# Optimization experiments

Measured on AMD Instinct MI355X. Metric: run time of the kernel, lower is better.

Reference implementation:

```python
import jax, jax.numpy as jnp
import numpy as np

N_NODES = 50000
N_EDGES = 800000
N_GRAPHS = 256
DIMS = [64, 128, 256, 512]
GRU_H = 256


def _linit(key, shape, fan_in):
    lim = 1.0 / np.sqrt(fan_in)
    return jax.random.uniform(key, shape, jnp.float32, -lim, lim)


def setup_inputs() -> dict:
    key = jax.random.key(0)
    ks = jax.random.split(key, 24)
    x = jax.random.normal(ks[0], (N_NODES, DIMS[0]), jnp.float32)
    edge_index = jax.random.randint(ks[1], (2, N_EDGES), 0, N_NODES, jnp.int64)
    batch_idx = jnp.sort(jax.random.randint(ks[2], (N_NODES,), 0, N_GRAPHS, jnp.int64))
    inp = {"x": x, "edge_index": edge_index, "batch_idx": batch_idx}
    # GCN layer weights (stored [in, out]) and biases
    for i in range(3):
        inp[f"gcn_w{i}"] = _linit(ks[3 + i], (DIMS[i], DIMS[i + 1]), DIMS[i])
        inp[f"gcn_b{i}"] = jnp.zeros((DIMS[i + 1],), jnp.float32)
    # gate nn: Linear(512, 1)
    inp["gate_w"] = _linit(ks[6], (DIMS[3], 1), DIMS[3])
    inp["gate_b"] = jnp.zeros((1,), jnp.float32)
    # GRU: 2 layers, torch layout W_ih [3H, in], W_hh [3H, H]
    ins = [DIMS[3], GRU_H]
    for l in range(2):
        inp[f"gru_wih{l}"] = _linit(ks[7 + 4 * l], (3 * GRU_H, ins[l]), GRU_H)
        inp[f"gru_whh{l}"] = _linit(ks[8 + 4 * l], (3 * GRU_H, GRU_H), GRU_H)
        inp[f"gru_bih{l}"] = _linit(ks[9 + 4 * l], (3 * GRU_H,), GRU_H)
        inp[f"gru_bhh{l}"] = _linit(ks[10 + 4 * l], (3 * GRU_H,), GRU_H)
    # output proj: Linear(256, 512), torch layout [out, in]
    inp["proj_w"] = _linit(ks[15], (DIMS[3], GRU_H), GRU_H)
    inp["proj_b"] = jnp.zeros((DIMS[3],), jnp.float32)
    return inp


def _gcn_norm(edge_index, n_nodes):
    # add self-loops, symmetric normalization (PyG GCNConv default)
    loop = jnp.arange(n_nodes, dtype=edge_index.dtype)
    src = jnp.concatenate([edge_index[0], loop])
    dst = jnp.concatenate([edge_index[1], loop])
    deg = jax.ops.segment_sum(jnp.ones_like(dst, jnp.float32), dst, num_segments=n_nodes)
    dinv = jnp.where(deg > 0, jax.lax.rsqrt(jnp.maximum(deg, 1.0)), 0.0)
    norm = dinv[src] * dinv[dst]
    return src, dst, norm


def _gru_cell(xv, h, wih, whh, bih, bhh):
    gi = xv @ wih.T + bih
    gh = h @ whh.T + bhh
    ir, iz, inn = jnp.split(gi, 3, axis=-1)
    hr, hz, hn = jnp.split(gh, 3, axis=-1)
    r = jax.nn.sigmoid(ir + hr)
    z = jax.nn.sigmoid(iz + hz)
    n = jnp.tanh(inn + r * hn)
    return (1.0 - z) * n + z * h


def reference(x, edge_index, batch_idx,
              gcn_w0, gcn_b0, gcn_w1, gcn_b1, gcn_w2, gcn_b2,
              gate_w, gate_b,
              gru_wih0, gru_whh0, gru_bih0, gru_bhh0,
              gru_wih1, gru_whh1, gru_bih1, gru_bhh1,
              proj_w, proj_b):
    n = x.shape[0]
    src, dst, norm = _gcn_norm(edge_index, n)
    for w, b in ((gcn_w0, gcn_b0), (gcn_w1, gcn_b1), (gcn_w2, gcn_b2)):
        h = x @ w                                  # [N, out]
        msg = h[src] * norm[:, None]               # gather over edges
        x = jax.ops.segment_sum(msg, dst, num_segments=n) + b
        x = jax.nn.relu(x)
    # attentional aggregation: segment softmax over gate scores
    gate = (x @ gate_w + gate_b)[:, 0]             # [N]
    gmax = jax.ops.segment_max(gate, batch_idx, num_segments=N_GRAPHS)
    e = jnp.exp(gate - gmax[batch_idx])
    denom = jax.ops.segment_sum(e, batch_idx, num_segments=N_GRAPHS)
    alpha = e / denom[batch_idx]
    graph_emb = jax.ops.segment_sum(x * alpha[:, None], batch_idx, num_segments=N_GRAPHS)  # [G, 512]
    # 2-layer GRU with seq_len=1, h0=0
    h0 = jnp.zeros((N_GRAPHS, GRU_H), x.dtype)
    h1 = _gru_cell(graph_emb, h0, gru_wih0, gru_whh0, gru_bih0, gru_bhh0)
    h2 = _gru_cell(h1, h0, gru_wih1, gru_whh1, gru_bih1, gru_bhh1)
    return h2 @ proj_w.T + proj_b                  # [G, 512]
```

## Files before the change

kernel.cpp:

```cpp
#include <hip/hip_runtime.h>


#define N_GRAPHS 256
#define GRU_H 256
#define SCAN_CHUNK 2048

typedef __attribute__((ext_vector_type(8))) short short8;
typedef __attribute__((ext_vector_type(4))) float floatx4;

typedef unsigned short ushort_t;
typedef unsigned int uint_t;

__device__ __forceinline__ float bflo(uint_t u) { return __uint_as_float(u << 16); }
__device__ __forceinline__ float bfhi(uint_t u) { return __uint_as_float(u & 0xffff0000u); }
__device__ __forceinline__ uint_t f2bf(float f) {
    uint_t u = __float_as_uint(f);
    return (u + 0x7fffu + ((u >> 16) & 1u)) >> 16;
}
__device__ __forceinline__ uint_t pack2(float a, float b) {
    return f2bf(a) | (f2bf(b) << 16);
}


__global__ void k_hist(const int* __restrict__ dst, int* __restrict__ counts, int E) {
    int e = blockIdx.x * blockDim.x + threadIdx.x;
    if (e < E) atomicAdd(&counts[dst[e]], 1);
}

__global__ __launch_bounds__(256) void k_scan1(const int* __restrict__ counts,
                                               int* __restrict__ rowptr,
                                               int* __restrict__ bsums,
                                               float* __restrict__ dinv, int n) {
    int b = blockIdx.x, t = threadIdx.x;
    int base = b * SCAN_CHUNK + t * 8;
    int v[8];
    int s = 0;
#pragma unroll
    for (int j = 0; j < 8; ++j) {
        int i = base + j;
        int c = (i < n) ? counts[i] : 0;
        v[j] = s;
        s += c;
        if (i < n) dinv[i] = rsqrtf((float)(c + 1));
    }
    __shared__ int sd[256];
    sd[t] = s;
    __syncthreads();
    for (int off = 1; off < 256; off <<= 1) {
        int tmp = (t >= off) ? sd[t - off] : 0;
        __syncthreads();
        sd[t] += tmp;
        __syncthreads();
    }
    int texcl = sd[t] - s;
    if (t == 255) bsums[b] = sd[255];
#pragma unroll
    for (int j = 0; j < 8; ++j) {
        int i = base + j;
        if (i < n) rowptr[i] = texcl + v[j];
    }
}

__global__ void k_scan2(int* __restrict__ bsums, int nb, int* __restrict__ rowptr, int n) {
    if (threadIdx.x == 0 && blockIdx.x == 0) {
        int run = 0;
        for (int b = 0; b < nb; ++b) { int t = bsums[b]; bsums[b] = run; run += t; }
        rowptr[n] = run;
    }
}

__global__ __launch_bounds__(256) void k_scan3(int* __restrict__ rowptr,
                                               int* __restrict__ cursor,
                                               const int* __restrict__ bsums, int n) {
    int b = blockIdx.x, t = threadIdx.x;
    int base = b * SCAN_CHUNK + t * 8;
    int off = bsums[b];
#pragma unroll
    for (int j = 0; j < 8; ++j) {
        int i = base + j;
        if (i < n) { int r = rowptr[i] + off; rowptr[i] = r; cursor[i] = r; }
    }
}

__global__ void k_fill(const int* __restrict__ src, const int* __restrict__ dst,
                       int* __restrict__ cursor, int* __restrict__ col, int E) {
    int e = blockIdx.x * blockDim.x + threadIdx.x;
    if (e < E) {
        int pos = atomicAdd(&cursor[dst[e]], 1);
        col[pos] = src[e];
    }
}


__global__ void k_wt(const float* __restrict__ W, ushort_t* __restrict__ Wt,
                     int K, int Nout, int shift ) {
    int idx = blockIdx.x * blockDim.x + threadIdx.x;
    if (idx >= K * Nout) return;
    int k = idx >> shift;
    int n = idx & (Nout - 1);
    Wt[(size_t)n * K + k] = (ushort_t)f2bf(W[idx]);
}


__global__ void k_split(const float* __restrict__ src, ushort_t* __restrict__ hi,
                        ushort_t* __restrict__ lo, int L) {
    int i = blockIdx.x * blockDim.x + threadIdx.x;
    if (i >= L) return;
    float v = src[i];
    uint_t h = f2bf(v);
    hi[i] = (ushort_t)h;
    lo[i] = (ushort_t)f2bf(v - __uint_as_float(h << 16));
}


__global__ void k_prescale(const float4* __restrict__ x, const float* __restrict__ dinv,
                           uint4* __restrict__ xs, int N) {
    int idx = blockIdx.x * blockDim.x + threadIdx.x;
    int n = idx >> 3;
    if (n >= N) return;
    float dn = dinv[n];
    float4 v0 = x[idx * 2], v1 = x[idx * 2 + 1];
    uint4 o;
    o.x = pack2(v0.x * dn, v0.y * dn);
    o.y = pack2(v0.z * dn, v0.w * dn);
    o.z = pack2(v1.x * dn, v1.y * dn);
    o.w = pack2(v1.z * dn, v1.w * dn);
    xs[idx] = o;
}


__device__ __forceinline__ void acc8(float& a0, float& a1, float& a2, float& a3,
                                     float& a4, float& a5, float& a6, float& a7,
                                     const uint4& v) {
    a0 += bflo(v.x); a1 += bfhi(v.x); a2 += bflo(v.y); a3 += bfhi(v.y);
    a4 += bflo(v.z); a5 += bfhi(v.z); a6 += bflo(v.w); a7 += bfhi(v.w);
}

__global__ void k_gather_bf16(const uint4* __restrict__ xs, const int* __restrict__ rp,
                              const int* __restrict__ col, const float* __restrict__ dinv,
                              uint4* __restrict__ agg, int N, int shift ) {
    int idx = blockIdx.x * blockDim.x + threadIdx.x;
    int n = idx >> shift;
    if (n >= N) return;
    int c = idx & ((1 << shift) - 1);
    int C8 = 1 << shift;
    int a = rp[n], b = rp[n + 1];
    uint4 u = xs[(size_t)n * C8 + c];
    float a0 = bflo(u.x), a1 = bfhi(u.x), a2 = bflo(u.y), a3 = bfhi(u.y);
    float a4 = bflo(u.z), a5 = bfhi(u.z), a6 = bflo(u.w), a7 = bfhi(u.w);
    int k = a;
    for (; k + 8 <= b; k += 8) {
        int ci[8];
#pragma unroll
        for (int j = 0; j < 8; ++j) ci[j] = col[k + j];
        uint4 v[8];
#pragma unroll
        for (int j = 0; j < 8; ++j) v[j] = xs[(size_t)ci[j] * C8 + c];
#pragma unroll
        for (int j = 0; j < 8; ++j)
            acc8(a0, a1, a2, a3, a4, a5, a6, a7, v[j]);
    }
    for (; k + 4 <= b; k += 4) {
        int ci[4];
#pragma unroll
        for (int j = 0; j < 4; ++j) ci[j] = col[k + j];
        uint4 v[4];
#pragma unroll
        for (int j = 0; j < 4; ++j) v[j] = xs[(size_t)ci[j] * C8 + c];
#pragma unroll
        for (int j = 0; j < 4; ++j)
            acc8(a0, a1, a2, a3, a4, a5, a6, a7, v[j]);
    }
    for (; k < b; ++k) {
        uint4 v = xs[(size_t)col[k] * C8 + c];
        acc8(a0, a1, a2, a3, a4, a5, a6, a7, v);
    }
    float dn = dinv[n];
    uint4 o;
    o.x = pack2(a0 * dn, a1 * dn);
    o.y = pack2(a2 * dn, a3 * dn);
    o.z = pack2(a4 * dn, a5 * dn);
    o.w = pack2(a6 * dn, a7 * dn);
    agg[idx] = o;
}


__global__ __launch_bounds__(256) void k_gemm_mfma(
    const ushort_t* __restrict__ A, const ushort_t* __restrict__ Wt,
    const float* __restrict__ bias, const float* __restrict__ dinv,
    ushort_t* __restrict__ C, int M, int K, int Nout, int scale_out) {
    __shared__ ushort_t As[64 * 72];
    __shared__ ushort_t Bs[64 * 72];
    int tid = threadIdx.x;
    int wave = tid >> 6, lane = tid & 63;
    int quad = lane >> 4, lr = lane & 15;
    int wm = (wave & 1) * 32, wn = (wave >> 1) * 32;
    int bm = blockIdx.x * 64, bn = blockIdx.y * 64;

    floatx4 zero = {0.f, 0.f, 0.f, 0.f};
    floatx4 acc00 = zero, acc01 = zero, acc10 = zero, acc11 = zero;

    int r0 = tid >> 3,         ko0 = (tid & 7) * 8;
    int r1 = (tid + 256) >> 3, ko1 = ((tid + 256) & 7) * 8;

    for (int k0 = 0; k0 < K; k0 += 64) {
        int ar0 = min(bm + r0, M - 1);
        int ar1 = min(bm + r1, M - 1);
        uint4 av0 = *(const uint4*)(A + (size_t)ar0 * K + k0 + ko0);
        uint4 av1 = *(const uint4*)(A + (size_t)ar1 * K + k0 + ko1);
        uint4 bv0 = *(const uint4*)(Wt + (size_t)(bn + r0) * K + k0 + ko0);
        uint4 bv1 = *(const uint4*)(Wt + (size_t)(bn + r1) * K + k0 + ko1);
        __syncthreads();
        *(uint4*)&As[r0 * 72 + ko0] = av0;
        *(uint4*)&As[r1 * 72 + ko1] = av1;
        *(uint4*)&Bs[r0 * 72 + ko0] = bv0;
        *(uint4*)&Bs[r1 * 72 + ko1] = bv1;
        __syncthreads();
#pragma unroll
        for (int ks = 0; ks < 2; ++ks) {
            short8 af0 = *(short8*)&As[(wm + lr) * 72 + ks * 32 + quad * 8];
            short8 af1 = *(short8*)&As[(wm + 16 + lr) * 72 + ks * 32 + quad * 8];
            short8 bf0 = *(short8*)&Bs[(wn + lr) * 72 + ks * 32 + quad * 8];
            short8 bf1 = *(short8*)&Bs[(wn + 16 + lr) * 72 + ks * 32 + quad * 8];
            acc00 = __builtin_amdgcn_mfma_f32_16x16x32_bf16(af0, bf0, acc00, 0, 0, 0);
            acc01 = __builtin_amdgcn_mfma_f32_16x16x32_bf16(af0, bf1, acc01, 0, 0, 0);
            acc10 = __builtin_amdgcn_mfma_f32_16x16x32_bf16(af1, bf0, acc10, 0, 0, 0);
            acc11 = __builtin_amdgcn_mfma_f32_16x16x32_bf16(af1, bf1, acc11, 0, 0, 0);
        }
    }

#pragma unroll
    for (int mi = 0; mi < 2; ++mi) {
#pragma unroll
        for (int ni = 0; ni < 2; ++ni) {
            floatx4 acc = (mi == 0) ? (ni == 0 ? acc00 : acc01)
                                    : (ni == 0 ? acc10 : acc11);
            int col = bn + wn + ni * 16 + lr;
            float bcol = bias[col];
#pragma unroll
            for (int r = 0; r < 4; ++r) {
                int row = bm + wm + mi * 16 + quad * 4 + r;
                if (row < M) {
                    float v = acc[r] + bcol;
                    v = fmaxf(v, 0.0f);
                    if (scale_out) v *= dinv[row];
                    C[(size_t)row * Nout + col] = (ushort_t)f2bf(v);
                }
            }
        }
    }
}


__global__ __launch_bounds__(256) void k_gemm3(
    const ushort_t* __restrict__ Ahi, const ushort_t* __restrict__ Alo,
    const ushort_t* __restrict__ Whi, const ushort_t* __restrict__ Wlo,
    const float* __restrict__ bias, float* __restrict__ C,
    int M, int K, int Nout) {
    __shared__ ushort_t AsH[64 * 72];
    __shared__ ushort_t AsL[64 * 72];
    __shared__ ushort_t BsH[64 * 72];
    __shared__ ushort_t BsL[64 * 72];
    int tid = threadIdx.x;
    int wave = tid >> 6, lane = tid & 63;
    int quad = lane >> 4, lr = lane & 15;
    int wm = (wave & 1) * 32, wn = (wave >> 1) * 32;
    int bm = blockIdx.x * 64, bn = blockIdx.y * 64;

    floatx4 zero = {0.f, 0.f, 0.f, 0.f};
    floatx4 acc00 = zero, acc01 = zero, acc10 = zero, acc11 = zero;

    int r0 = tid >> 3,         ko0 = (tid & 7) * 8;
    int r1 = (tid + 256) >> 3, ko1 = ((tid + 256) & 7) * 8;

    for (int k0 = 0; k0 < K; k0 += 64) {
        int ar0 = min(bm + r0, M - 1);
        int ar1 = min(bm + r1, M - 1);
        size_t a0o = (size_t)ar0 * K + k0 + ko0, a1o = (size_t)ar1 * K + k0 + ko1;
        size_t b0o = (size_t)(bn + r0) * K + k0 + ko0, b1o = (size_t)(bn + r1) * K + k0 + ko1;
        uint4 ah0 = *(const uint4*)(Ahi + a0o), ah1 = *(const uint4*)(Ahi + a1o);
        uint4 al0 = *(const uint4*)(Alo + a0o), al1 = *(const uint4*)(Alo + a1o);
        uint4 bh0 = *(const uint4*)(Whi + b0o), bh1 = *(const uint4*)(Whi + b1o);
        uint4 bl0 = *(const uint4*)(Wlo + b0o), bl1 = *(const uint4*)(Wlo + b1o);
        __syncthreads();
        *(uint4*)&AsH[r0 * 72 + ko0] = ah0; *(uint4*)&AsH[r1 * 72 + ko1] = ah1;
        *(uint4*)&AsL[r0 * 72 + ko0] = al0; *(uint4*)&AsL[r1 * 72 + ko1] = al1;
        *(uint4*)&BsH[r0 * 72 + ko0] = bh0; *(uint4*)&BsH[r1 * 72 + ko1] = bh1;
        *(uint4*)&BsL[r0 * 72 + ko0] = bl0; *(uint4*)&BsL[r1 * 72 + ko1] = bl1;
        __syncthreads();
#pragma unroll
        for (int ks = 0; ks < 2; ++ks) {
            int a0i = (wm + lr) * 72 + ks * 32 + quad * 8;
            int a1i = (wm + 16 + lr) * 72 + ks * 32 + quad * 8;
            int b0i = (wn + lr) * 72 + ks * 32 + quad * 8;
            int b1i = (wn + 16 + lr) * 72 + ks * 32 + quad * 8;
            short8 afh0 = *(short8*)&AsH[a0i], afh1 = *(short8*)&AsH[a1i];
            short8 afl0 = *(short8*)&AsL[a0i], afl1 = *(short8*)&AsL[a1i];
            short8 bfh0 = *(short8*)&BsH[b0i], bfh1 = *(short8*)&BsH[b1i];
            short8 bfl0 = *(short8*)&BsL[b0i], bfl1 = *(short8*)&BsL[b1i];
            acc00 = __builtin_amdgcn_mfma_f32_16x16x32_bf16(afh0, bfh0, acc00, 0, 0, 0);
            acc00 = __builtin_amdgcn_mfma_f32_16x16x32_bf16(afh0, bfl0, acc00, 0, 0, 0);
            acc00 = __builtin_amdgcn_mfma_f32_16x16x32_bf16(afl0, bfh0, acc00, 0, 0, 0);
            acc01 = __builtin_amdgcn_mfma_f32_16x16x32_bf16(afh0, bfh1, acc01, 0, 0, 0);
            acc01 = __builtin_amdgcn_mfma_f32_16x16x32_bf16(afh0, bfl1, acc01, 0, 0, 0);
            acc01 = __builtin_amdgcn_mfma_f32_16x16x32_bf16(afl0, bfh1, acc01, 0, 0, 0);
            acc10 = __builtin_amdgcn_mfma_f32_16x16x32_bf16(afh1, bfh0, acc10, 0, 0, 0);
            acc10 = __builtin_amdgcn_mfma_f32_16x16x32_bf16(afh1, bfl0, acc10, 0, 0, 0);
            acc10 = __builtin_amdgcn_mfma_f32_16x16x32_bf16(afl1, bfh0, acc10, 0, 0, 0);
            acc11 = __builtin_amdgcn_mfma_f32_16x16x32_bf16(afh1, bfh1, acc11, 0, 0, 0);
            acc11 = __builtin_amdgcn_mfma_f32_16x16x32_bf16(afh1, bfl1, acc11, 0, 0, 0);
            acc11 = __builtin_amdgcn_mfma_f32_16x16x32_bf16(afl1, bfh1, acc11, 0, 0, 0);
        }
    }

#pragma unroll
    for (int mi = 0; mi < 2; ++mi) {
#pragma unroll
        for (int ni = 0; ni < 2; ++ni) {
            floatx4 acc = (mi == 0) ? (ni == 0 ? acc00 : acc01)
                                    : (ni == 0 ? acc10 : acc11);
            int col = bn + wn + ni * 16 + lr;
            float bcol = bias ? bias[col] : 0.0f;
#pragma unroll
            for (int r = 0; r < 4; ++r) {
                int row = bm + wm + mi * 16 + quad * 4 + r;
                if (row < M)
                    C[(size_t)row * Nout + col] = acc[r] + bcol;
            }
        }
    }
}


__global__ void k_gru_ep(const float* __restrict__ gi, const float* __restrict__ bih,
                         const float* __restrict__ bhh,
                         ushort_t* __restrict__ hhi, ushort_t* __restrict__ hlo, int G) {
    int idx = blockIdx.x * blockDim.x + threadIdx.x;
    int g = idx >> 8, j = idx & 255;
    if (g >= G) return;
    const float* row = gi + (size_t)g * 768;
    float ir = row[j]       + bih[j]       + bhh[j];
    float iz = row[j + 256] + bih[j + 256] + bhh[j + 256];
    float in = row[j + 512] + bih[j + 512];
    float r = 1.0f / (1.0f + expf(-ir));
    float z = 1.0f / (1.0f + expf(-iz));
    float nn = tanhf(in + r * bhh[j + 512]);
    float h = (1.0f - z) * nn;
    uint_t hi = f2bf(h);
    hhi[idx] = (ushort_t)hi;
    hlo[idx] = (ushort_t)f2bf(h - __uint_as_float(hi << 16));
}


__global__ void k_gate(const uint4* __restrict__ x, const float4* __restrict__ gw,
                       const float* __restrict__ gb, float* __restrict__ gate, int N) {
    int gid = blockIdx.x * blockDim.x + threadIdx.x;
    int wave = gid >> 6;
    int lane = gid & 63;
    if (wave >= N) return;
    uint4 u = x[(size_t)wave * 64 + lane];
    float4 w0 = gw[lane * 2], w1 = gw[lane * 2 + 1];
    float acc = bflo(u.x) * w0.x + bfhi(u.x) * w0.y + bflo(u.y) * w0.z + bfhi(u.y) * w0.w
              + bflo(u.z) * w1.x + bfhi(u.z) * w1.y + bflo(u.w) * w1.z + bfhi(u.w) * w1.w;
#pragma unroll
    for (int off = 32; off > 0; off >>= 1) acc += __shfl_down(acc, off, 64);
    if (lane == 0) gate[wave] = acc + gb[0];
}


__global__ void k_gstart(const int* __restrict__ batch, int* __restrict__ gstart,
                         int N, int G) {
    int g = blockIdx.x * blockDim.x + threadIdx.x;
    if (g > G) return;
    if (g == G) { gstart[G] = N; return; }
    int lo = 0, hi = N;
    while (lo < hi) {
        int mid = (lo + hi) >> 1;
        if (batch[mid] < g) lo = mid + 1; else hi = mid;
    }
    gstart[g] = lo;
}


__global__ __launch_bounds__(256) void k_softmax_emb(
    const uint_t* __restrict__ x , const float* __restrict__ gate,
    const int* __restrict__ gstart, float* __restrict__ emb) {
    int g = blockIdx.x;
    int s = gstart[g], e = gstart[g + 1];
    __shared__ float red[256];
    __shared__ float sal[256];
    int tid = threadIdx.x;
    float m = -INFINITY;
    for (int i = s + tid; i < e; i += 256) m = fmaxf(m, gate[i]);
    red[tid] = m; __syncthreads();
    for (int off = 128; off > 0; off >>= 1) {
        if (tid < off) red[tid] = fmaxf(red[tid], red[tid + off]);
        __syncthreads();
    }
    m = red[0]; __syncthreads();
    float ssum = 0.f;
    for (int i = s + tid; i < e; i += 256) ssum += expf(gate[i] - m);
    red[tid] = ssum; __syncthreads();
    for (int off = 128; off > 0; off >>= 1) {
        if (tid < off) red[tid] += red[tid + off];
        __syncthreads();
    }
    float denom = red[0];
    float inv = (denom > 0.f) ? 1.0f / denom : 0.0f;
    float acc0 = 0.f, acc1 = 0.f;
    for (int base = s; base < e; base += 256) {
        int i = base + tid;
        __syncthreads();
        sal[tid] = (i < e) ? expf(gate[i] - m) * inv : 0.0f;
        __syncthreads();
        int cnt = min(256, e - base);
        for (int k = 0; k < cnt; ++k) {
            float a = sal[k];
            uint_t u = x[(size_t)(base + k) * 256 + tid];
            acc0 += a * bflo(u);
            acc1 += a * bfhi(u);
        }
    }
    emb[(size_t)g * 512 + tid * 2]     = acc0;
    emb[(size_t)g * 512 + tid * 2 + 1] = acc1;
}


extern "C" void kernel_launch(void* const* d_in, const int* in_sizes, int n_in,
                              void* d_out, int out_size, void* d_ws, size_t ws_size,
                              hipStream_t stream) {
    const float* x       = (const float*)d_in[0];
    const int*   ei      = (const int*)d_in[1];
    const int*   batch   = (const int*)d_in[2];
    const float* w0      = (const float*)d_in[3];
    const float* b0      = (const float*)d_in[4];
    const float* w1      = (const float*)d_in[5];
    const float* b1      = (const float*)d_in[6];
    const float* w2      = (const float*)d_in[7];
    const float* b2      = (const float*)d_in[8];
    const float* gate_w  = (const float*)d_in[9];
    const float* gate_b  = (const float*)d_in[10];
    const float* wih0    = (const float*)d_in[11];
    const float* bih0    = (const float*)d_in[13];
    const float* bhh0    = (const float*)d_in[14];
    const float* wih1    = (const float*)d_in[15];
    const float* bih1    = (const float*)d_in[17];
    const float* bhh1    = (const float*)d_in[18];
    const float* pw      = (const float*)d_in[19];
    const float* pb      = (const float*)d_in[20];
    float* out = (float*)d_out;

    const int N = in_sizes[2];
    const int E = in_sizes[1] / 2;
    const int G = N_GRAPHS;

    char* base = (char*)d_ws;
    size_t off = 0;
    auto alloc = [&](size_t bytes) -> char* {
        char* p = base + off;
        off = (off + bytes + 255) & ~(size_t)255;
        return p;
    };
    ushort_t* bufA  = (ushort_t*)alloc((size_t)N * 512 * 2);
    ushort_t* bufB  = (ushort_t*)alloc((size_t)N * 512 * 2);
    float* dinv     = (float*)alloc((size_t)N * 4);
    float* gateArr  = (float*)alloc((size_t)N * 4);
    int*   counts   = (int*)alloc((size_t)(N + 1) * 4);
    int*   cursor   = (int*)alloc((size_t)(N + 1) * 4);
    int*   rowptr   = (int*)alloc((size_t)(N + 1) * 4);
    int*   bsums    = (int*)alloc((size_t)256 * 4);
    int*   col      = (int*)alloc((size_t)E * 4);
    int*   gstart   = (int*)alloc((size_t)(G + 1) * 4);
    float* emb      = (float*)alloc((size_t)G * 512 * 4);
    ushort_t* wt0   = (ushort_t*)alloc((size_t)128 * 64 * 2);
    ushort_t* wt1   = (ushort_t*)alloc((size_t)256 * 128 * 2);
    ushort_t* wt2   = (ushort_t*)alloc((size_t)512 * 256 * 2);
    ushort_t* ih0H  = (ushort_t*)alloc((size_t)768 * 512 * 2);
    ushort_t* ih0L  = (ushort_t*)alloc((size_t)768 * 512 * 2);
    ushort_t* ih1H  = (ushort_t*)alloc((size_t)768 * 256 * 2);
    ushort_t* ih1L  = (ushort_t*)alloc((size_t)768 * 256 * 2);
    ushort_t* pwH   = (ushort_t*)alloc((size_t)512 * 256 * 2);
    ushort_t* pwL   = (ushort_t*)alloc((size_t)512 * 256 * 2);
    ushort_t* embH  = (ushort_t*)alloc((size_t)G * 512 * 2);
    ushort_t* embL  = (ushort_t*)alloc((size_t)G * 512 * 2);
    ushort_t* h1H   = (ushort_t*)alloc((size_t)G * 256 * 2);
    ushort_t* h1L   = (ushort_t*)alloc((size_t)G * 256 * 2);
    ushort_t* h2H   = (ushort_t*)alloc((size_t)G * 256 * 2);
    ushort_t* h2L   = (ushort_t*)alloc((size_t)G * 256 * 2);
    float* gi       = (float*)alloc((size_t)G * 768 * 4);
    (void)ws_size; (void)n_in; (void)out_size;

    const int* src = ei;
    const int* dst = ei + E;

    const int nb = (N + SCAN_CHUNK - 1) / SCAN_CHUNK;

    hipMemsetAsync(counts, 0, (size_t)(N + 1) * 4, stream);
    k_hist<<<(E + 255) / 256, 256, 0, stream>>>(dst, counts, E);
    k_scan1<<<nb, 256, 0, stream>>>(counts, rowptr, bsums, dinv, N);
    k_scan2<<<1, 64, 0, stream>>>(bsums, nb, rowptr, N);
    k_scan3<<<nb, 256, 0, stream>>>(rowptr, cursor, bsums, N);
    k_fill<<<(E + 255) / 256, 256, 0, stream>>>(src, dst, cursor, col, E);
    k_wt<<<(64 * 128 + 255) / 256, 256, 0, stream>>>(w0, wt0, 64, 128, 7);
    k_wt<<<(128 * 256 + 255) / 256, 256, 0, stream>>>(w1, wt1, 128, 256, 8);
    k_wt<<<(256 * 512 + 255) / 256, 256, 0, stream>>>(w2, wt2, 256, 512, 9);
    k_split<<<(768 * 512 + 255) / 256, 256, 0, stream>>>(wih0, ih0H, ih0L, 768 * 512);
    k_split<<<(768 * 256 + 255) / 256, 256, 0, stream>>>(wih1, ih1H, ih1L, 768 * 256);
    k_split<<<(512 * 256 + 255) / 256, 256, 0, stream>>>(pw, pwH, pwL, 512 * 256);

    int mBlocks = (N + 63) / 64;

    k_prescale<<<(N * 8 + 255) / 256, 256, 0, stream>>>((const float4*)x, dinv, (uint4*)bufA, N);
    k_gather_bf16<<<(N * 8 + 255) / 256, 256, 0, stream>>>((const uint4*)bufA, rowptr, col, dinv, (uint4*)bufB, N, 3);
    k_gemm_mfma<<<dim3(mBlocks, 2), 256, 0, stream>>>(bufB, wt0, b0, dinv, bufA, N, 64, 128, 1);

    k_gather_bf16<<<(N * 16 + 255) / 256, 256, 0, stream>>>((const uint4*)bufA, rowptr, col, dinv, (uint4*)bufB, N, 4);
    k_gemm_mfma<<<dim3(mBlocks, 4), 256, 0, stream>>>(bufB, wt1, b1, dinv, bufA, N, 128, 256, 1);

    k_gather_bf16<<<(N * 32 + 255) / 256, 256, 0, stream>>>((const uint4*)bufA, rowptr, col, dinv, (uint4*)bufB, N, 5);
    k_gemm_mfma<<<dim3(mBlocks, 8), 256, 0, stream>>>(bufB, wt2, b2, dinv, bufA, N, 256, 512, 0);

    k_gate<<<(N * 64 + 255) / 256, 256, 0, stream>>>((const uint4*)bufA, (const float4*)gate_w, gate_b, gateArr, N);
    k_gstart<<<1, 512, 0, stream>>>(batch, gstart, N, G);
    k_softmax_emb<<<G, 256, 0, stream>>>((const uint_t*)bufA, gateArr, gstart, emb);

    k_split<<<(G * 512 + 255) / 256, 256, 0, stream>>>(emb, embH, embL, G * 512);
    k_gemm3<<<dim3(G / 64, 12), 256, 0, stream>>>(embH, embL, ih0H, ih0L, nullptr, gi, G, 512, 768);
    k_gru_ep<<<G, 256, 0, stream>>>(gi, bih0, bhh0, h1H, h1L, G);

    k_gemm3<<<dim3(G / 64, 12), 256, 0, stream>>>(h1H, h1L, ih1H, ih1L, nullptr, gi, G, 256, 768);
    k_gru_ep<<<G, 256, 0, stream>>>(gi, bih1, bhh1, h2H, h2L, G);

    k_gemm3<<<dim3(G / 64, 8), 256, 0, stream>>>(h2H, h2L, pwH, pwL, pb, out, G, 256, 512);
}
```

Before: 461.6 us.

## Fuse gate projection into last GEMM epilogue and merge small setup kernels

Computes the attention gate dot product inside the final GCN GEMM epilogue, reducing across lanes with shuffles and accumulating per-row partials into a zeroed gate array with atomics. The separate gate and graph-start kernels go away, with graph bounds found by binary search inside the softmax kernel, which now writes the hi/lo bf16 split directly. The scan's second pass is folded into the third, and the weight conversion and split launches are merged into single kernels, all to cut launch count and one re-read of the 50000x512 activation. In exchange the gate uses fp32 atomics (non-deterministic order), the gate bias is dropped on the assumption it cancels in the softmax, and the memset relies on the workspace layout placing gateArr before counts.

```diff
diff --git a/kernel.cpp b/kernel.cpp
--- a/kernel.cpp
+++ b/kernel.cpp
@@ -61,20 +61,25 @@
     }
 }
 
-__global__ void k_scan2(int* __restrict__ bsums, int nb, int* __restrict__ rowptr, int n) {
-    if (threadIdx.x == 0 && blockIdx.x == 0) {
-        int run = 0;
-        for (int b = 0; b < nb; ++b) { int t = bsums[b]; bsums[b] = run; run += t; }
-        rowptr[n] = run;
-    }
-}
-
 __global__ __launch_bounds__(256) void k_scan3(int* __restrict__ rowptr,
                                                int* __restrict__ cursor,
-                                               const int* __restrict__ bsums, int n) {
+                                               const int* __restrict__ bsums,
+                                               int n, int nb) {
     int b = blockIdx.x, t = threadIdx.x;
+    __shared__ int s_off;
+    if (t == 0) {
+        int off = 0, tot = 0;
+        for (int i = 0; i < nb; ++i) {
+            int v = bsums[i];
+            if (i < b) off += v;
+            tot += v;
+        }
+        s_off = off;
+        if (b == 0) rowptr[n] = tot;
+    }
+    __syncthreads();
+    int off = s_off;
     int base = b * SCAN_CHUNK + t * 8;
-    int off = bsums[b];
 #pragma unroll
     for (int j = 0; j < 8; ++j) {
         int i = base + j;
@@ -92,24 +97,40 @@
 }
 
 
-__global__ void k_wt(const float* __restrict__ W, ushort_t* __restrict__ Wt,
-                     int K, int Nout, int shift ) {
+__global__ void k_wt_all(const float* __restrict__ w0, const float* __restrict__ w1,
+                         const float* __restrict__ w2, ushort_t* __restrict__ wt0,
+                         ushort_t* __restrict__ wt1, ushort_t* __restrict__ wt2) {
     int idx = blockIdx.x * blockDim.x + threadIdx.x;
-    if (idx >= K * Nout) return;
-    int k = idx >> shift;
-    int n = idx & (Nout - 1);
-    Wt[(size_t)n * K + k] = (ushort_t)f2bf(W[idx]);
-}
-
-
-__global__ void k_split(const float* __restrict__ src, ushort_t* __restrict__ hi,
-                        ushort_t* __restrict__ lo, int L) {
-    int i = blockIdx.x * blockDim.x + threadIdx.x;
-    if (i >= L) return;
-    float v = src[i];
+    if (idx < 8192) {
+        int k = idx >> 7, n = idx & 127;
+        wt0[(size_t)n * 64 + k] = (ushort_t)f2bf(w0[idx]);
+    } else if (idx < 40960) {
+        int i = idx - 8192;
+        int k = i >> 8, n = i & 255;
+        wt1[(size_t)n * 128 + k] = (ushort_t)f2bf(w1[i]);
+    } else if (idx < 172032) {
+        int i = idx - 40960;
+        int k = i >> 9, n = i & 511;
+        wt2[(size_t)n * 256 + k] = (ushort_t)f2bf(w2[i]);
+    }
+}
+
+
+__global__ void k_split_all(const float* __restrict__ wih0, const float* __restrict__ wih1,
+                            const float* __restrict__ pw,
+                            ushort_t* __restrict__ h0, ushort_t* __restrict__ l0,
+                            ushort_t* __restrict__ h1, ushort_t* __restrict__ l1,
+                            ushort_t* __restrict__ h2, ushort_t* __restrict__ l2) {
+    int idx = blockIdx.x * blockDim.x + threadIdx.x;
+    const float* s; ushort_t* H; ushort_t* L; int i;
+    if (idx < 393216)      { s = wih0; H = h0; L = l0; i = idx; }
+    else if (idx < 589824) { s = wih1; H = h1; L = l1; i = idx - 393216; }
+    else if (idx < 720896) { s = pw;   H = h2; L = l2; i = idx - 589824; }
+    else return;
+    float v = s[i];
     uint_t h = f2bf(v);
-    hi[i] = (ushort_t)h;
-    lo[i] = (ushort_t)f2bf(v - __uint_as_float(h << 16));
+    H[i] = (ushort_t)h;
+    L[i] = (ushort_t)f2bf(v - __uint_as_float(h << 16));
 }
 
 
@@ -188,7 +209,8 @@
 __global__ __launch_bounds__(256) void k_gemm_mfma(
     const ushort_t* __restrict__ A, const ushort_t* __restrict__ Wt,
     const float* __restrict__ bias, const float* __restrict__ dinv,
-    ushort_t* __restrict__ C, int M, int K, int Nout, int scale_out) {
+    ushort_t* __restrict__ C, int M, int K, int Nout, int scale_out,
+    const float* __restrict__ gate_w, float* __restrict__ gateArr) {
     __shared__ ushort_t As[64 * 72];
     __shared__ ushort_t Bs[64 * 72];
     int tid = threadIdx.x;
@@ -229,6 +251,12 @@
         }
     }
 
+    float gwv[2] = {0.f, 0.f};
+    if (gate_w) {
+        gwv[0] = gate_w[bn + wn + lr];
+        gwv[1] = gate_w[bn + wn + 16 + lr];
+    }
+    float pg[2][4] = {};
 #pragma unroll
     for (int mi = 0; mi < 2; ++mi) {
 #pragma unroll
@@ -243,8 +271,26 @@
                 if (row < M) {
                     float v = acc[r] + bcol;
                     v = fmaxf(v, 0.0f);
+                    if (gate_w) pg[mi][r] += v * gwv[ni];
                     if (scale_out) v *= dinv[row];
                     C[(size_t)row * Nout + col] = (ushort_t)f2bf(v);
+                }
+            }
+        }
+    }
+    if (gate_w) {
+#pragma unroll
+        for (int mi = 0; mi < 2; ++mi) {
+#pragma unroll
+            for (int r = 0; r < 4; ++r) {
+                float p = pg[mi][r];
+                p += __shfl_down(p, 8, 16);
+                p += __shfl_down(p, 4, 16);
+                p += __shfl_down(p, 2, 16);
+                p += __shfl_down(p, 1, 16);
+                if (lr == 0) {
+                    int row = bm + wm + mi * 16 + quad * 4 + r;
+                    if (row < M) atomicAdd(&gateArr[row], p);
                 }
             }
         }
@@ -352,41 +398,20 @@
 }
 
 
-__global__ void k_gate(const uint4* __restrict__ x, const float4* __restrict__ gw,
-                       const float* __restrict__ gb, float* __restrict__ gate, int N) {
-    int gid = blockIdx.x * blockDim.x + threadIdx.x;
-    int wave = gid >> 6;
-    int lane = gid & 63;
-    if (wave >= N) return;
-    uint4 u = x[(size_t)wave * 64 + lane];
-    float4 w0 = gw[lane * 2], w1 = gw[lane * 2 + 1];
-    float acc = bflo(u.x) * w0.x + bfhi(u.x) * w0.y + bflo(u.y) * w0.z + bfhi(u.y) * w0.w
-              + bflo(u.z) * w1.x + bfhi(u.z) * w1.y + bflo(u.w) * w1.z + bfhi(u.w) * w1.w;
-#pragma unroll
-    for (int off = 32; off > 0; off >>= 1) acc += __shfl_down(acc, off, 64);
-    if (lane == 0) gate[wave] = acc + gb[0];
-}
-
-
-__global__ void k_gstart(const int* __restrict__ batch, int* __restrict__ gstart,
-                         int N, int G) {
-    int g = blockIdx.x * blockDim.x + threadIdx.x;
-    if (g > G) return;
-    if (g == G) { gstart[G] = N; return; }
-    int lo = 0, hi = N;
-    while (lo < hi) {
-        int mid = (lo + hi) >> 1;
-        if (batch[mid] < g) lo = mid + 1; else hi = mid;
-    }
-    gstart[g] = lo;
-}
-
-
 __global__ __launch_bounds__(256) void k_softmax_emb(
     const uint_t* __restrict__ x , const float* __restrict__ gate,
-    const int* __restrict__ gstart, float* __restrict__ emb) {
+    const int* __restrict__ batch, int N,
+    ushort_t* __restrict__ embH, ushort_t* __restrict__ embL) {
     int g = blockIdx.x;
-    int s = gstart[g], e = gstart[g + 1];
+    int s, e;
+    {
+        int lo = 0, hi = N;
+        while (lo < hi) { int mid = (lo + hi) >> 1; if (batch[mid] < g) lo = mid + 1; else hi = mid; }
+        s = lo;
+        lo = s; hi = N;
+        while (lo < hi) { int mid = (lo + hi) >> 1; if (batch[mid] < g + 1) lo = mid + 1; else hi = mid; }
+        e = lo;
+    }
     __shared__ float red[256];
     __shared__ float sal[256];
     int tid = threadIdx.x;
@@ -421,8 +446,13 @@
             acc1 += a * bfhi(u);
         }
     }
-    emb[(size_t)g * 512 + tid * 2]     = acc0;
-    emb[(size_t)g * 512 + tid * 2 + 1] = acc1;
+    int i0 = g * 512 + tid * 2;
+    uint_t h0 = f2bf(acc0);
+    uint_t h1 = f2bf(acc1);
+    embH[i0]     = (ushort_t)h0;
+    embH[i0 + 1] = (ushort_t)h1;
+    embL[i0]     = (ushort_t)f2bf(acc0 - __uint_as_float(h0 << 16));
+    embL[i0 + 1] = (ushort_t)f2bf(acc1 - __uint_as_float(h1 << 16));
 }
 
 
@@ -439,7 +469,6 @@
     const float* w2      = (const float*)d_in[7];
     const float* b2      = (const float*)d_in[8];
     const float* gate_w  = (const float*)d_in[9];
-    const float* gate_b  = (const float*)d_in[10];
     const float* wih0    = (const float*)d_in[11];
     const float* bih0    = (const float*)d_in[13];
     const float* bhh0    = (const float*)d_in[14];
@@ -470,8 +499,6 @@
     int*   rowptr   = (int*)alloc((size_t)(N + 1) * 4);
     int*   bsums    = (int*)alloc((size_t)256 * 4);
     int*   col      = (int*)alloc((size_t)E * 4);
-    int*   gstart   = (int*)alloc((size_t)(G + 1) * 4);
-    float* emb      = (float*)alloc((size_t)G * 512 * 4);
     ushort_t* wt0   = (ushort_t*)alloc((size_t)128 * 64 * 2);
     ushort_t* wt1   = (ushort_t*)alloc((size_t)256 * 128 * 2);
     ushort_t* wt2   = (ushort_t*)alloc((size_t)512 * 256 * 2);
@@ -495,36 +522,31 @@
 
     const int nb = (N + SCAN_CHUNK - 1) / SCAN_CHUNK;
 
-    hipMemsetAsync(counts, 0, (size_t)(N + 1) * 4, stream);
+    size_t zbytes = (size_t)((char*)counts - (char*)gateArr) + (size_t)(N + 1) * 4;
+    hipMemsetAsync(gateArr, 0, zbytes, stream);
+
     k_hist<<<(E + 255) / 256, 256, 0, stream>>>(dst, counts, E);
     k_scan1<<<nb, 256, 0, stream>>>(counts, rowptr, bsums, dinv, N);
-    k_scan2<<<1, 64, 0, stream>>>(bsums, nb, rowptr, N);
-    k_scan3<<<nb, 256, 0, stream>>>(rowptr, cursor, bsums, N);
+    k_scan3<<<nb, 256, 0, stream>>>(rowptr, cursor, bsums, N, nb);
     k_fill<<<(E + 255) / 256, 256, 0, stream>>>(src, dst, cursor, col, E);
-    k_wt<<<(64 * 128 + 255) / 256, 256, 0, stream>>>(w0, wt0, 64, 128, 7);
-    k_wt<<<(128 * 256 + 255) / 256, 256, 0, stream>>>(w1, wt1, 128, 256, 8);
-    k_wt<<<(256 * 512 + 255) / 256, 256, 0, stream>>>(w2, wt2, 256, 512, 9);
-    k_split<<<(768 * 512 + 255) / 256, 256, 0, stream>>>(wih0, ih0H, ih0L, 768 * 512);
-    k_split<<<(768 * 256 + 255) / 256, 256, 0, stream>>>(wih1, ih1H, ih1L, 768 * 256);
-    k_split<<<(512 * 256 + 255) / 256, 256, 0, stream>>>(pw, pwH, pwL, 512 * 256);
+    k_wt_all<<<(172032 + 255) / 256, 256, 0, stream>>>(w0, w1, w2, wt0, wt1, wt2);
+    k_split_all<<<(720896 + 255) / 256, 256, 0, stream>>>(wih0, wih1, pw,
+                                                          ih0H, ih0L, ih1H, ih1L, pwH, pwL);
 
     int mBlocks = (N + 63) / 64;
 
     k_prescale<<<(N * 8 + 255) / 256, 256, 0, stream>>>((const float4*)x, dinv, (uint4*)bufA, N);
     k_gather_bf16<<<(N * 8 + 255) / 256, 256, 0, stream>>>((const uint4*)bufA, rowptr, col, dinv, (uint4*)bufB, N, 3);
-    k_gemm_mfma<<<dim3(mBlocks, 2), 256, 0, stream>>>(bufB, wt0, b0, dinv, bufA, N, 64, 128, 1);
+    k_gemm_mfma<<<dim3(mBlocks, 2), 256, 0, stream>>>(bufB, wt0, b0, dinv, bufA, N, 64, 128, 1, nullptr, nullptr);
 
     k_gather_bf16<<<(N * 16 + 255) / 256, 256, 0, stream>>>((const uint4*)bufA, rowptr, col, dinv, (uint4*)bufB, N, 4);
-    k_gemm_mfma<<<dim3(mBlocks, 4), 256, 0, stream>>>(bufB, wt1, b1, dinv, bufA, N, 128, 256, 1);
+    k_gemm_mfma<<<dim3(mBlocks, 4), 256, 0, stream>>>(bufB, wt1, b1, dinv, bufA, N, 128, 256, 1, nullptr, nullptr);
 
     k_gather_bf16<<<(N * 32 + 255) / 256, 256, 0, stream>>>((const uint4*)bufA, rowptr, col, dinv, (uint4*)bufB, N, 5);
-    k_gemm_mfma<<<dim3(mBlocks, 8), 256, 0, stream>>>(bufB, wt2, b2, dinv, bufA, N, 256, 512, 0);
-
-    k_gate<<<(N * 64 + 255) / 256, 256, 0, stream>>>((const uint4*)bufA, (const float4*)gate_w, gate_b, gateArr, N);
-    k_gstart<<<1, 512, 0, stream>>>(batch, gstart, N, G);
-    k_softmax_emb<<<G, 256, 0, stream>>>((const uint_t*)bufA, gateArr, gstart, emb);
-
-    k_split<<<(G * 512 + 255) / 256, 256, 0, stream>>>(emb, embH, embL, G * 512);
+    k_gemm_mfma<<<dim3(mBlocks, 8), 256, 0, stream>>>(bufB, wt2, b2, dinv, bufA, N, 256, 512, 0, gate_w, gateArr);
+
+    k_softmax_emb<<<G, 256, 0, stream>>>((const uint_t*)bufA, gateArr, batch, N, embH, embL);
+
     k_gemm3<<<dim3(G / 64, 12), 256, 0, stream>>>(embH, embL, ih0H, ih0L, nullptr, gi, G, 512, 768);
     k_gru_ep<<<G, 256, 0, stream>>>(gi, bih0, bhh0, h1H, h1L, G);
 
```

Measured after the change: 446.8 us. -3.2%, faster.
